# Kernel optimization log

Measured on AMD Instinct MI355X. Metric: run time of the kernel, lower is better.

## Reference

```python
import jax, jax.numpy as jnp
import numpy as np

NUM_FEATURES = 16
EMBED_DIM = 8
D = NUM_FEATURES * EMBED_DIM  # 128
BATCH = 524288


def setup_inputs() -> dict:
    key = jax.random.key(0)
    ks = jax.random.split(key, 7)
    s = 1.0 / np.sqrt(D)
    return {
        "x": jax.random.normal(ks[0], (BATCH, D), dtype=jnp.float32),
        "Wk": jax.random.normal(ks[1], (D, D), dtype=jnp.float32) * s,
        "bk": jnp.zeros((D,), dtype=jnp.float32),
        "Wq": jax.random.normal(ks[2], (D, D), dtype=jnp.float32) * s,
        "bq": jnp.zeros((D,), dtype=jnp.float32),
        "Wv": jax.random.normal(ks[3], (D, D), dtype=jnp.float32) * s,
        "bv": jnp.zeros((D,), dtype=jnp.float32),
    }


def reference(x, Wk, bk, Wq, bq, Wv, bv):
    # Dense + exact gelu projections (keras 'gelu' activation is exact erf-gelu)
    gelu = lambda t: jax.nn.gelu(t, approximate=False)
    k = gelu(x @ Wk + bk)  # [B, D]
    q = gelu(x @ Wq + bq)
    v = gelu(x @ Wv + bv)
    B = x.shape[0]
    k = k.reshape(B, NUM_FEATURES, EMBED_DIM)
    q = q.reshape(B, NUM_FEATURES, EMBED_DIM)
    v = v.reshape(B, NUM_FEATURES, EMBED_DIM)
    # y = K^T Q : [B, E, E]; res = V y : [B, F, E]
    y = jnp.einsum('bfe,bfg->beg', k, q)
    res = jnp.einsum('bfe,beg->bfg', v, y)
    return res.reshape(B, D) + x
```

## Files before the change

### kernel.cpp

```cpp
#include <hip/hip_runtime.h>

typedef __bf16 bf16x8 __attribute__((ext_vector_type(8)));
typedef float f32x4 __attribute__((ext_vector_type(4)));
typedef float f32x2 __attribute__((ext_vector_type(2)));
typedef __fp16 fp16x2 __attribute__((ext_vector_type(2)));
typedef unsigned short ushort8 __attribute__((ext_vector_type(8)));
typedef unsigned int uint4v __attribute__((ext_vector_type(4)));
typedef unsigned int uint2v __attribute__((ext_vector_type(2)));

__device__ __forceinline__ unsigned short f2bf(float f){
    unsigned u = __float_as_uint(f);
    u += 0x7fffu + ((u >> 16) & 1u);
    return (unsigned short)(u >> 16);
}
__device__ __forceinline__ unsigned cvt_pk_bf16(float lo, float hi){
    unsigned r;
    asm("v_cvt_pk_bf16_f32 %0, %1, %2" : "=v"(r) : "v"(lo), "v"(hi));
    return r;
}
__device__ __forceinline__ unsigned cvt_pk_f16(float lo, float hi){
    return __builtin_bit_cast(unsigned, __builtin_amdgcn_cvt_pkrtz(lo, hi));
}
__device__ __forceinline__ float fdot2(unsigned a, unsigned b, float c){
#if __has_builtin(__builtin_amdgcn_fdot2)
    return __builtin_amdgcn_fdot2(__builtin_bit_cast(fp16x2, a),
                                  __builtin_bit_cast(fp16x2, b), c, false);
#else
    float d;
    asm("v_dot2_f32_f16 %0, %1, %2, %3" : "=v"(d) : "v"(a), "v"(b), "v"(c));
    return d;
#endif
}
__device__ __forceinline__ float bflo(unsigned w){ return __uint_as_float(w << 16); }
__device__ __forceinline__ float bfhi(unsigned w){ return __uint_as_float(w & 0xffff0000u); }

__device__ __forceinline__ float gelu_poly(float x){
    float t = x * x;
    float h = fmaf(fmaf(fmaf(fmaf(2.66044e-5f, t, -7.46798e-4f), t,
                             9.014181e-3f), t, -6.5889388e-2f), t, 0.39894228f);
    float p = fmaf(x, h, 0.5f);
    p = fminf(fmaxf(p, 0.0f), 1.0f);
    return x * p;
}

#define TM 64
#define LST 136

__global__ void pack_w_kernel(const float* __restrict__ Wk, const float* __restrict__ Wq,
                              const float* __restrict__ Wv, unsigned short* __restrict__ wp){
    int b = blockIdx.x;
    int lane = threadIdx.x;
    int p  = b >> 5;
    int ks = (b >> 3) & 3;
    int nf = b & 7;
    const float* W = (p == 0) ? Wk : ((p == 1) ? Wq : Wv);
    int k0  = ks * 32 + (lane >> 4) * 8;
    int col = nf * 16 + (lane & 15);
    unsigned short* dst = wp + ((size_t)b * 64 + lane) * 8;
    #pragma unroll
    for (int j = 0; j < 8; ++j) dst[j] = f2bf(W[(size_t)(k0 + j) * 128 + col]);
}

__global__ __launch_bounds__(256, 3) void fused_tcross(
        const float* __restrict__ x, const unsigned short* __restrict__ wp,
        const float* __restrict__ bk, const float* __restrict__ bq,
        const float* __restrict__ bv, float* __restrict__ out){
    __shared__ __align__(16) unsigned short smem[3 * TM * LST];

    const int tid  = threadIdx.x;
    const int lane = tid & 63;
    const int wave = tid >> 6;
    const int c16  = lane & 15;
    const int kg   = lane >> 4;
    const long long row0 = (long long)blockIdx.x * TM;

    float bpre0[2], bpre1[2], bpre2[2];
    #pragma unroll
    for (int j = 0; j < 2; ++j){
        int col = (wave * 2 + j) * 16 + c16;
        bpre0[j] = bv[col];
        bpre1[j] = bq[col];
        bpre2[j] = bk[col];
    }

    const float* xblk = x + row0 * 128;
    f32x4 resid[8];
    #pragma unroll
    for (int it = 0; it < 8; ++it){
        int e = tid * 4 + it * 1024;
        f32x4 v = *(const f32x4*)(xblk + e);
        resid[it] = v;
        uint2v w;
        w[0] = cvt_pk_bf16(v[0], v[1]);
        w[1] = cvt_pk_bf16(v[2], v[3]);
        *(uint2v*)&smem[(e >> 7) * LST + (e & 127)] = w;
    }
    __syncthreads();

    const int pack_p[3] = {2, 1, 0};
    const int plane[3]  = {2, 1, 0};
    #pragma unroll 1
    for (int pi = 0; pi < 3; ++pi){
        f32x4 acc[4][2];
        const f32x4 zero = {0.f, 0.f, 0.f, 0.f};
        #pragma unroll
        for (int m = 0; m < 4; ++m){ acc[m][0] = zero; acc[m][1] = zero; }
        #pragma unroll
        for (int ks = 0; ks < 4; ++ks){
            bf16x8 af[4];
            #pragma unroll
            for (int m = 0; m < 4; ++m)
                af[m] = __builtin_bit_cast(bf16x8,
                    *(const ushort8*)&smem[(m * 16 + c16) * LST + ks * 32 + kg * 8]);
            #pragma unroll
            for (int j = 0; j < 2; ++j){
                const int nf = wave * 2 + j;
                const size_t fidx = ((size_t)((pack_p[pi] * 4 + ks) * 8 + nf) * 64 + lane) * 8;
                bf16x8 wfrag = __builtin_bit_cast(bf16x8, *(const ushort8*)(wp + fidx));
                #pragma unroll
                for (int m = 0; m < 4; ++m)
                    acc[m][j] = __builtin_amdgcn_mfma_f32_16x16x32_bf16(
                        af[m], wfrag, acc[m][j], 0, 0, 0);
            }
        }
        if (pi == 2) __syncthreads();
        unsigned short* sp = smem + plane[pi] * TM * LST;
        const float bb0 = (pi == 0) ? bpre0[0] : ((pi == 1) ? bpre1[0] : bpre2[0]);
        const float bb1 = (pi == 0) ? bpre0[1] : ((pi == 1) ? bpre1[1] : bpre2[1]);
        #pragma unroll
        for (int j = 0; j < 2; ++j){
            const int col = (wave * 2 + j) * 16 + c16;
            const float bb = j ? bb1 : bb0;
            #pragma unroll
            for (int m = 0; m < 4; ++m){
                float g0 = gelu_poly(acc[m][j][0] + bb);
                float g1 = gelu_poly(acc[m][j][1] + bb);
                float g2 = gelu_poly(acc[m][j][2] + bb);
                float g3 = gelu_poly(acc[m][j][3] + bb);
                unsigned u01 = (pi == 0) ? cvt_pk_f16(g0, g1) : cvt_pk_bf16(g0, g1);
                unsigned u23 = (pi == 0) ? cvt_pk_f16(g2, g3) : cvt_pk_bf16(g2, g3);
                const int r = m * 16 + kg * 4;
                sp[(r + 0) * LST + col] = (unsigned short)u01;
                sp[(r + 1) * LST + col] = (unsigned short)(u01 >> 16);
                sp[(r + 2) * LST + col] = (unsigned short)u23;
                sp[(r + 3) * LST + col] = (unsigned short)(u23 >> 16);
            }
        }
    }
    __syncthreads();

    const int row = tid >> 2;
    const int sub = tid & 3;
    const unsigned short* krow = smem + 0 * TM * LST + row * LST;
    const unsigned short* qrow = smem + 1 * TM * LST + row * LST;
    const unsigned short* vrow = smem + 2 * TM * LST + row * LST;

    f32x2 y2[8];
    #pragma unroll
    for (int e = 0; e < 8; ++e) y2[e] = (f32x2){0.f, 0.f};
    #pragma unroll
    for (int f = 0; f < 16; ++f){
        uint4v ku = *(const uint4v*)(krow + f * 8);
        unsigned qw = *(const unsigned*)(qrow + f * 8 + sub * 2);
        f32x2 qq = {bflo(qw), bfhi(qw)};
        float kf[8] = {bflo(ku[0]), bfhi(ku[0]), bflo(ku[1]), bfhi(ku[1]),
                       bflo(ku[2]), bfhi(ku[2]), bflo(ku[3]), bfhi(ku[3])};
        #pragma unroll
        for (int e = 0; e < 8; ++e){
            f32x2 kk = {kf[e], kf[e]};
            y2[e] += kk * qq;
        }
    }
    unsigned yp0[4], yp1[4];
    #pragma unroll
    for (int i = 0; i < 4; ++i){
        yp0[i] = cvt_pk_f16(y2[2*i][0], y2[2*i+1][0]);
        yp1[i] = cvt_pk_f16(y2[2*i][1], y2[2*i+1][1]);
    }
    f32x2 rr[16];
    #pragma unroll
    for (int f = 0; f < 16; ++f){
        uint4v vv = *(const uint4v*)(vrow + f * 8);
        float a0 = 0.f, a1 = 0.f;
        #pragma unroll
        for (int i = 0; i < 4; ++i){
            a0 = fdot2(vv[i], yp0[i], a0);
            a1 = fdot2(vv[i], yp1[i], a1);
        }
        rr[f] = (f32x2){a0, a1};
    }
    __syncthreads();

    float* s_res = (float*)smem;
    #pragma unroll
    for (int f = 0; f < 16; ++f)
        *(f32x2*)&s_res[row * LST + f * 8 + sub * 2] = rr[f];
    __syncthreads();

    float* outb = out + row0 * 128;
    #pragma unroll
    for (int it = 0; it < 8; ++it){
        int e = tid * 4 + it * 1024;
        f32x4 rv = *(const f32x4*)&s_res[(e >> 7) * LST + (e & 127)];
        rv += resid[it];
        *(f32x4*)(outb + e) = rv;
    }
}

extern "C" void kernel_launch(void* const* d_in, const int* in_sizes, int n_in,
                              void* d_out, int out_size, void* d_ws, size_t ws_size,
                              hipStream_t stream){
    const float* x  = (const float*)d_in[0];
    const float* Wk = (const float*)d_in[1];
    const float* bk = (const float*)d_in[2];
    const float* Wq = (const float*)d_in[3];
    const float* bq = (const float*)d_in[4];
    const float* Wv = (const float*)d_in[5];
    const float* bv = (const float*)d_in[6];
    float* out = (float*)d_out;
    unsigned short* wp = (unsigned short*)d_ws;

    const int B = in_sizes[0] / 128;

    pack_w_kernel<<<96, 64, 0, stream>>>(Wk, Wq, Wv, wp);
    fused_tcross<<<B / TM, 256, 0, stream>>>(x, wp, bk, bq, bv, out);

    (void)n_in; (void)out_size; (void)ws_size;
}
```

Baseline: 168.9 us.

## Use 512-thread blocks splitting projection MFMA tiles across 8 waves

Doubles the block to 8 waves, so each wave computes a 32x32 output tile (2x2 MFMA fragments) of each projection instead of 64x32. Residual load and store are spread over 512 threads, while the tensor-cross stage still runs on only the first 256 threads. The aim is more waves in flight and less register pressure per wave during the MFMA and GELU phase. In exchange, half the waves sit idle during the cross stage, and the 4-blocks-per-CU launch bound may be limited by LDS usage.

```diff
diff --git a/kernel.cpp b/kernel.cpp
--- a/kernel.cpp
+++ b/kernel.cpp
@@ -61,7 +61,7 @@
     for (int j = 0; j < 8; ++j) dst[j] = f2bf(W[(size_t)(k0 + j) * 128 + col]);
 }
 
-__global__ __launch_bounds__(256, 3) void fused_tcross(
+__global__ __launch_bounds__(512, 4) void fused_tcross(
         const float* __restrict__ x, const unsigned short* __restrict__ wp,
         const float* __restrict__ bk, const float* __restrict__ bq,
         const float* __restrict__ bv, float* __restrict__ out){
@@ -72,22 +72,24 @@
     const int wave = tid >> 6;
     const int c16  = lane & 15;
     const int kg   = lane >> 4;
+    const int wm   = wave & 1;
+    const int wn   = wave >> 1;
     const long long row0 = (long long)blockIdx.x * TM;
 
-    float bpre0[2], bpre1[2], bpre2[2];
-    #pragma unroll
-    for (int j = 0; j < 2; ++j){
-        int col = (wave * 2 + j) * 16 + c16;
-        bpre0[j] = bv[col];
-        bpre1[j] = bq[col];
-        bpre2[j] = bk[col];
+    float bpv[2], bpq[2], bpk[2];
+    #pragma unroll
+    for (int jj = 0; jj < 2; ++jj){
+        int col = (2 * wn + jj) * 16 + c16;
+        bpv[jj] = bv[col];
+        bpq[jj] = bq[col];
+        bpk[jj] = bk[col];
     }
 
     const float* xblk = x + row0 * 128;
-    f32x4 resid[8];
-    #pragma unroll
-    for (int it = 0; it < 8; ++it){
-        int e = tid * 4 + it * 1024;
+    f32x4 resid[4];
+    #pragma unroll
+    for (int it = 0; it < 4; ++it){
+        int e = tid * 4 + it * 2048;
         f32x4 v = *(const f32x4*)(xblk + e);
         resid[it] = v;
         uint2v w;
@@ -97,49 +99,45 @@
     }
     __syncthreads();
 
-    const int pack_p[3] = {2, 1, 0};
-    const int plane[3]  = {2, 1, 0};
     #pragma unroll 1
     for (int pi = 0; pi < 3; ++pi){
-        f32x4 acc[4][2];
+        const int pp = 2 - pi;
+        f32x4 acc[2][2];
         const f32x4 zero = {0.f, 0.f, 0.f, 0.f};
-        #pragma unroll
-        for (int m = 0; m < 4; ++m){ acc[m][0] = zero; acc[m][1] = zero; }
+        acc[0][0] = zero; acc[0][1] = zero; acc[1][0] = zero; acc[1][1] = zero;
         #pragma unroll
         for (int ks = 0; ks < 4; ++ks){
-            bf16x8 af[4];
-            #pragma unroll
-            for (int m = 0; m < 4; ++m)
-                af[m] = __builtin_bit_cast(bf16x8,
-                    *(const ushort8*)&smem[(m * 16 + c16) * LST + ks * 32 + kg * 8]);
-            #pragma unroll
-            for (int j = 0; j < 2; ++j){
-                const int nf = wave * 2 + j;
-                const size_t fidx = ((size_t)((pack_p[pi] * 4 + ks) * 8 + nf) * 64 + lane) * 8;
-                bf16x8 wfrag = __builtin_bit_cast(bf16x8, *(const ushort8*)(wp + fidx));
+            bf16x8 af[2];
+            #pragma unroll
+            for (int mm = 0; mm < 2; ++mm)
+                af[mm] = __builtin_bit_cast(bf16x8, *(const ushort8*)
+                    &smem[((2 * wm + mm) * 16 + c16) * LST + ks * 32 + kg * 8]);
+            #pragma unroll
+            for (int jj = 0; jj < 2; ++jj){
+                const int nf = 2 * wn + jj;
+                const size_t fidx = ((size_t)((pp * 4 + ks) * 8 + nf) * 64 + lane) * 8;
+                bf16x8 wf = __builtin_bit_cast(bf16x8, *(const ushort8*)(wp + fidx));
                 #pragma unroll
-                for (int m = 0; m < 4; ++m)
-                    acc[m][j] = __builtin_amdgcn_mfma_f32_16x16x32_bf16(
-                        af[m], wfrag, acc[m][j], 0, 0, 0);
+                for (int mm = 0; mm < 2; ++mm)
+                    acc[mm][jj] = __builtin_amdgcn_mfma_f32_16x16x32_bf16(
+                        af[mm], wf, acc[mm][jj], 0, 0, 0);
             }
         }
         if (pi == 2) __syncthreads();
-        unsigned short* sp = smem + plane[pi] * TM * LST;
-        const float bb0 = (pi == 0) ? bpre0[0] : ((pi == 1) ? bpre1[0] : bpre2[0]);
-        const float bb1 = (pi == 0) ? bpre0[1] : ((pi == 1) ? bpre1[1] : bpre2[1]);
-        #pragma unroll
-        for (int j = 0; j < 2; ++j){
-            const int col = (wave * 2 + j) * 16 + c16;
-            const float bb = j ? bb1 : bb0;
-            #pragma unroll
-            for (int m = 0; m < 4; ++m){
-                float g0 = gelu_poly(acc[m][j][0] + bb);
-                float g1 = gelu_poly(acc[m][j][1] + bb);
-                float g2 = gelu_poly(acc[m][j][2] + bb);
-                float g3 = gelu_poly(acc[m][j][3] + bb);
+        unsigned short* sp = smem + (2 - pi) * TM * LST;
+        #pragma unroll
+        for (int jj = 0; jj < 2; ++jj){
+            const int col = (2 * wn + jj) * 16 + c16;
+            const float bb = (pi == 0) ? bpv[jj] : ((pi == 1) ? bpq[jj] : bpk[jj]);
+            #pragma unroll
+            for (int mm = 0; mm < 2; ++mm){
+                float g0 = gelu_poly(acc[mm][jj][0] + bb);
+                float g1 = gelu_poly(acc[mm][jj][1] + bb);
+                float g2 = gelu_poly(acc[mm][jj][2] + bb);
+                float g3 = gelu_poly(acc[mm][jj][3] + bb);
                 unsigned u01 = (pi == 0) ? cvt_pk_f16(g0, g1) : cvt_pk_bf16(g0, g1);
                 unsigned u23 = (pi == 0) ? cvt_pk_f16(g2, g3) : cvt_pk_bf16(g2, g3);
-                const int r = m * 16 + kg * 4;
+                const int r = (2 * wm + mm) * 16 + kg * 4;
                 sp[(r + 0) * LST + col] = (unsigned short)u01;
                 sp[(r + 1) * LST + col] = (unsigned short)(u01 >> 16);
                 sp[(r + 2) * LST + col] = (unsigned short)u23;
@@ -151,56 +149,60 @@
 
     const int row = tid >> 2;
     const int sub = tid & 3;
-    const unsigned short* krow = smem + 0 * TM * LST + row * LST;
-    const unsigned short* qrow = smem + 1 * TM * LST + row * LST;
-    const unsigned short* vrow = smem + 2 * TM * LST + row * LST;
-
-    f32x2 y2[8];
-    #pragma unroll
-    for (int e = 0; e < 8; ++e) y2[e] = (f32x2){0.f, 0.f};
-    #pragma unroll
-    for (int f = 0; f < 16; ++f){
-        uint4v ku = *(const uint4v*)(krow + f * 8);
-        unsigned qw = *(const unsigned*)(qrow + f * 8 + sub * 2);
-        f32x2 qq = {bflo(qw), bfhi(qw)};
-        float kf[8] = {bflo(ku[0]), bfhi(ku[0]), bflo(ku[1]), bfhi(ku[1]),
-                       bflo(ku[2]), bfhi(ku[2]), bflo(ku[3]), bfhi(ku[3])};
-        #pragma unroll
-        for (int e = 0; e < 8; ++e){
-            f32x2 kk = {kf[e], kf[e]};
-            y2[e] += kk * qq;
-        }
-    }
-    unsigned yp0[4], yp1[4];
-    #pragma unroll
-    for (int i = 0; i < 4; ++i){
-        yp0[i] = cvt_pk_f16(y2[2*i][0], y2[2*i+1][0]);
-        yp1[i] = cvt_pk_f16(y2[2*i][1], y2[2*i+1][1]);
-    }
     f32x2 rr[16];
-    #pragma unroll
-    for (int f = 0; f < 16; ++f){
-        uint4v vv = *(const uint4v*)(vrow + f * 8);
-        float a0 = 0.f, a1 = 0.f;
+    if (tid < 256){
+        const unsigned short* krow = smem + 0 * TM * LST + row * LST;
+        const unsigned short* qrow = smem + 1 * TM * LST + row * LST;
+        const unsigned short* vrow = smem + 2 * TM * LST + row * LST;
+
+        f32x2 y2[8];
+        #pragma unroll
+        for (int e = 0; e < 8; ++e) y2[e] = (f32x2){0.f, 0.f};
+        #pragma unroll
+        for (int f = 0; f < 16; ++f){
+            uint4v ku = *(const uint4v*)(krow + f * 8);
+            unsigned qw = *(const unsigned*)(qrow + f * 8 + sub * 2);
+            f32x2 qq = {bflo(qw), bfhi(qw)};
+            float kf[8] = {bflo(ku[0]), bfhi(ku[0]), bflo(ku[1]), bfhi(ku[1]),
+                           bflo(ku[2]), bfhi(ku[2]), bflo(ku[3]), bfhi(ku[3])};
+            #pragma unroll
+            for (int e = 0; e < 8; ++e){
+                f32x2 kk = {kf[e], kf[e]};
+                y2[e] += kk * qq;
+            }
+        }
+        unsigned yp0[4], yp1[4];
         #pragma unroll
         for (int i = 0; i < 4; ++i){
-            a0 = fdot2(vv[i], yp0[i], a0);
-            a1 = fdot2(vv[i], yp1[i], a1);
-        }
-        rr[f] = (f32x2){a0, a1};
+            yp0[i] = cvt_pk_f16(y2[2*i][0], y2[2*i+1][0]);
+            yp1[i] = cvt_pk_f16(y2[2*i][1], y2[2*i+1][1]);
+        }
+        #pragma unroll
+        for (int f = 0; f < 16; ++f){
+            uint4v vv = *(const uint4v*)(vrow + f * 8);
+            float a0 = 0.f, a1 = 0.f;
+            #pragma unroll
+            for (int i = 0; i < 4; ++i){
+                a0 = fdot2(vv[i], yp0[i], a0);
+                a1 = fdot2(vv[i], yp1[i], a1);
+            }
+            rr[f] = (f32x2){a0, a1};
+        }
     }
     __syncthreads();
 
     float* s_res = (float*)smem;
-    #pragma unroll
-    for (int f = 0; f < 16; ++f)
-        *(f32x2*)&s_res[row * LST + f * 8 + sub * 2] = rr[f];
+    if (tid < 256){
+        #pragma unroll
+        for (int f = 0; f < 16; ++f)
+            *(f32x2*)&s_res[row * LST + f * 8 + sub * 2] = rr[f];
+    }
     __syncthreads();
 
     float* outb = out + row0 * 128;
     #pragma unroll
-    for (int it = 0; it < 8; ++it){
-        int e = tid * 4 + it * 1024;
+    for (int it = 0; it < 4; ++it){
+        int e = tid * 4 + it * 2048;
         f32x4 rv = *(const f32x4*)&s_res[(e >> 7) * LST + (e & 127)];
         rv += resid[it];
         *(f32x4*)(outb + e) = rv;
@@ -223,7 +225,7 @@
     const int B = in_sizes[0] / 128;
 
     pack_w_kernel<<<96, 64, 0, stream>>>(Wk, Wq, Wv, wp);
-    fused_tcross<<<B / TM, 256, 0, stream>>>(x, wp, bk, bq, bv, out);
+    fused_tcross<<<B / TM, 512, 0, stream>>>(x, wp, bk, bq, bv, out);
 
     (void)n_in; (void)out_size; (void)ws_size;
 }
```

After: 176.2 us. +4.3%, slower.

## Assign each wave full row strips for projections and drop block barriers

Applied to the files above, without the earlier changes.

The work split of the three projection GEMMs changes. Before, each wave computed all 64 rows for 32 output columns; now each wave computes its own 16 rows across all 128 columns. The wave's A fragments are loaded from LDS once and kept in registers for all three projections. Because each wave now writes and later reads only its own rows, two __syncthreads are removed and K/Q/V are written to planes in natural order (V stays f16). In exchange, each wave reads four times as many packed weight fragments from global/L2, and accumulator register use rises.

```diff
diff --git a/kernel.cpp b/kernel.cpp
--- a/kernel.cpp
+++ b/kernel.cpp
@@ -45,6 +45,7 @@
 
 #define TM 64
 #define LST 136
+#define PLANE (TM * LST)
 
 __global__ void pack_w_kernel(const float* __restrict__ Wk, const float* __restrict__ Wq,
                               const float* __restrict__ Wv, unsigned short* __restrict__ wp){
@@ -65,7 +66,7 @@
         const float* __restrict__ x, const unsigned short* __restrict__ wp,
         const float* __restrict__ bk, const float* __restrict__ bq,
         const float* __restrict__ bv, float* __restrict__ out){
-    __shared__ __align__(16) unsigned short smem[3 * TM * LST];
+    __shared__ __align__(16) unsigned short smem[3 * PLANE];
 
     const int tid  = threadIdx.x;
     const int lane = tid & 63;
@@ -74,13 +75,13 @@
     const int kg   = lane >> 4;
     const long long row0 = (long long)blockIdx.x * TM;
 
-    float bpre0[2], bpre1[2], bpre2[2];
-    #pragma unroll
-    for (int j = 0; j < 2; ++j){
-        int col = (wave * 2 + j) * 16 + c16;
-        bpre0[j] = bv[col];
-        bpre1[j] = bq[col];
-        bpre2[j] = bk[col];
+    float bpk[8], bpq[8], bpv[8];
+    #pragma unroll
+    for (int nf = 0; nf < 8; ++nf){
+        int col = nf * 16 + c16;
+        bpk[nf] = bk[col];
+        bpq[nf] = bq[col];
+        bpv[nf] = bv[col];
     }
 
     const float* xblk = x + row0 * 128;
@@ -97,63 +98,53 @@
     }
     __syncthreads();
 
-    const int pack_p[3] = {2, 1, 0};
-    const int plane[3]  = {2, 1, 0};
+    bf16x8 af[4];
+    #pragma unroll
+    for (int ks = 0; ks < 4; ++ks)
+        af[ks] = __builtin_bit_cast(bf16x8,
+            *(const ushort8*)&smem[(wave * 16 + c16) * LST + ks * 32 + kg * 8]);
+
     #pragma unroll 1
     for (int pi = 0; pi < 3; ++pi){
-        f32x4 acc[4][2];
+        f32x4 acc[8];
         const f32x4 zero = {0.f, 0.f, 0.f, 0.f};
         #pragma unroll
-        for (int m = 0; m < 4; ++m){ acc[m][0] = zero; acc[m][1] = zero; }
+        for (int nf = 0; nf < 8; ++nf) acc[nf] = zero;
         #pragma unroll
         for (int ks = 0; ks < 4; ++ks){
-            bf16x8 af[4];
             #pragma unroll
-            for (int m = 0; m < 4; ++m)
-                af[m] = __builtin_bit_cast(bf16x8,
-                    *(const ushort8*)&smem[(m * 16 + c16) * LST + ks * 32 + kg * 8]);
-            #pragma unroll
-            for (int j = 0; j < 2; ++j){
-                const int nf = wave * 2 + j;
-                const size_t fidx = ((size_t)((pack_p[pi] * 4 + ks) * 8 + nf) * 64 + lane) * 8;
+            for (int nf = 0; nf < 8; ++nf){
+                const size_t fidx = ((size_t)((pi * 4 + ks) * 8 + nf) * 64 + lane) * 8;
                 bf16x8 wfrag = __builtin_bit_cast(bf16x8, *(const ushort8*)(wp + fidx));
-                #pragma unroll
-                for (int m = 0; m < 4; ++m)
-                    acc[m][j] = __builtin_amdgcn_mfma_f32_16x16x32_bf16(
-                        af[m], wfrag, acc[m][j], 0, 0, 0);
+                acc[nf] = __builtin_amdgcn_mfma_f32_16x16x32_bf16(
+                    af[ks], wfrag, acc[nf], 0, 0, 0);
             }
         }
-        if (pi == 2) __syncthreads();
-        unsigned short* sp = smem + plane[pi] * TM * LST;
-        const float bb0 = (pi == 0) ? bpre0[0] : ((pi == 1) ? bpre1[0] : bpre2[0]);
-        const float bb1 = (pi == 0) ? bpre0[1] : ((pi == 1) ? bpre1[1] : bpre2[1]);
-        #pragma unroll
-        for (int j = 0; j < 2; ++j){
-            const int col = (wave * 2 + j) * 16 + c16;
-            const float bb = j ? bb1 : bb0;
-            #pragma unroll
-            for (int m = 0; m < 4; ++m){
-                float g0 = gelu_poly(acc[m][j][0] + bb);
-                float g1 = gelu_poly(acc[m][j][1] + bb);
-                float g2 = gelu_poly(acc[m][j][2] + bb);
-                float g3 = gelu_poly(acc[m][j][3] + bb);
-                unsigned u01 = (pi == 0) ? cvt_pk_f16(g0, g1) : cvt_pk_bf16(g0, g1);
-                unsigned u23 = (pi == 0) ? cvt_pk_f16(g2, g3) : cvt_pk_bf16(g2, g3);
-                const int r = m * 16 + kg * 4;
-                sp[(r + 0) * LST + col] = (unsigned short)u01;
-                sp[(r + 1) * LST + col] = (unsigned short)(u01 >> 16);
-                sp[(r + 2) * LST + col] = (unsigned short)u23;
-                sp[(r + 3) * LST + col] = (unsigned short)(u23 >> 16);
-            }
-        }
-    }
-    __syncthreads();
+        unsigned short* sp = smem + pi * PLANE;
+        const float* bp = (pi == 0) ? bpk : ((pi == 1) ? bpq : bpv);
+        const int rbase = wave * 16 + kg * 4;
+        #pragma unroll
+        for (int nf = 0; nf < 8; ++nf){
+            const int col = nf * 16 + c16;
+            const float bb = bp[nf];
+            float g0 = gelu_poly(acc[nf][0] + bb);
+            float g1 = gelu_poly(acc[nf][1] + bb);
+            float g2 = gelu_poly(acc[nf][2] + bb);
+            float g3 = gelu_poly(acc[nf][3] + bb);
+            unsigned u01 = (pi == 2) ? cvt_pk_f16(g0, g1) : cvt_pk_bf16(g0, g1);
+            unsigned u23 = (pi == 2) ? cvt_pk_f16(g2, g3) : cvt_pk_bf16(g2, g3);
+            sp[(rbase + 0) * LST + col] = (unsigned short)u01;
+            sp[(rbase + 1) * LST + col] = (unsigned short)(u01 >> 16);
+            sp[(rbase + 2) * LST + col] = (unsigned short)u23;
+            sp[(rbase + 3) * LST + col] = (unsigned short)(u23 >> 16);
+        }
+    }
 
     const int row = tid >> 2;
     const int sub = tid & 3;
-    const unsigned short* krow = smem + 0 * TM * LST + row * LST;
-    const unsigned short* qrow = smem + 1 * TM * LST + row * LST;
-    const unsigned short* vrow = smem + 2 * TM * LST + row * LST;
+    const unsigned short* krow = smem + 0 * PLANE + row * LST;
+    const unsigned short* qrow = smem + 1 * PLANE + row * LST;
+    const unsigned short* vrow = smem + 2 * PLANE + row * LST;
 
     f32x2 y2[8];
     #pragma unroll
```

After: 331.2 us. +96.1%, slower.
